# Kernel tuning notes

Hardware: AMD Instinct MI355X
Metric: run time of the kernel (lower is better)

## Reference

```python
import jax, jax.numpy as jnp
import numpy as np

F = 50          # num features
CARD = 10000    # cardinality per feature
D = 64          # factor_dim
A = 64          # attention_size
IU, JU = np.triu_indices(F, k=1)  # upper-triangular pair indices, P = F*(F-1)/2


def setup_inputs() -> dict:
    key = jax.random.key(0)
    ks = jax.random.split(key, 8)
    inputs = jax.random.randint(ks[0], (1024, F), 0, CARD, dtype=jnp.int32)
    emb_table = jax.random.normal(ks[1], (F * CARD, D), dtype=jnp.float32) * 0.05
    w_lin = jax.random.normal(ks[2], (F * CARD,), dtype=jnp.float32) * 0.05
    b_lin = jnp.zeros((1,), dtype=jnp.float32)
    W1 = jax.random.normal(ks[3], (D, A), dtype=jnp.float32) * (1.0 / np.sqrt(D))
    b1 = jnp.zeros((A,), dtype=jnp.float32)
    W2 = jax.random.normal(ks[4], (A, 1), dtype=jnp.float32) * (1.0 / np.sqrt(A))
    b2 = jnp.zeros((1,), dtype=jnp.float32)
    return {"inputs": inputs, "emb_table": emb_table, "w_lin": w_lin,
            "b_lin": b_lin, "W1": W1, "b1": b1, "W2": W2, "b2": b2}


def reference(inputs, emb_table, w_lin, b_lin, W1, b1, W2, b2):
    # Per-feature tables are stacked into one flat table; offset indices per feature.
    flat_idx = inputs + (jnp.arange(F, dtype=jnp.int32) * CARD)[None, :]  # [B, F]
    line_out = jnp.sum(w_lin[flat_idx], axis=1, keepdims=True) + b_lin    # [B, 1]
    factor = emb_table[flat_idx]                                          # [B, F, D]
    # Upper-triangular pairwise element-wise products (i < j), P = F(F-1)/2
    inter = factor[:, IU, :] * factor[:, JU, :]                           # [B, P, D]
    # Attention: Dense(A) -> ReLU -> Dense(1) -> Softmax over pairs
    h = jax.nn.relu(jnp.einsum('bpd,da->bpa', inter, W1) + b1)            # [B, P, A]
    logits = jnp.einsum('bpa,ao->bpo', h, W2) + b2                        # [B, P, 1]
    scores = jax.nn.softmax(logits, axis=1)                               # [B, P, 1]
    pooled = jnp.sum(inter, axis=-1, keepdims=True)                       # [B, P, 1]
    return line_out + jnp.sum(pooled * scores, axis=1)                    # [B, 1]
```

## Files before the change

kernel.cpp:

```cpp
#include <hip/hip_runtime.h>
#include <math.h>

#define FN 50
#define CARD 10000
#define NP 1225
#define NTILE 77
#define NPAD (NTILE*16)
#define FSTRIDE 72

typedef _Float16 half8 __attribute__((ext_vector_type(8)));
typedef __fp16 half2t __attribute__((ext_vector_type(2)));
typedef float floatx4 __attribute__((ext_vector_type(4)));

static __device__ __forceinline__ half2t h2max0(half2t v) {
  half2t r;
  r[0] = v[0] > (__fp16)0 ? v[0] : (__fp16)0;
  r[1] = v[1] > (__fp16)0 ? v[1] : (__fp16)0;
  return r;
}
static __device__ __forceinline__ float hdot2(half2t a, half2t b, float c) {
#if __has_builtin(__builtin_amdgcn_fdot2)
  return __builtin_amdgcn_fdot2(a, b, c, false);
#else
  return c + (float)a[0]*(float)b[0] + (float)a[1]*(float)b[1];
#endif
}

__global__ __launch_bounds__(256, 4)
void afm_kernel(const int* __restrict__ inp,
                const float* __restrict__ emb,
                const float* __restrict__ wlin,
                const float* __restrict__ blin,
                const float* __restrict__ W1,
                const float* __restrict__ b1,
                const float* __restrict__ W2,
                const float* __restrict__ b2,
                float* __restrict__ out)
{
  __shared__ __align__(16) _Float16 s_fac[FN][FSTRIDE];
  __shared__ __align__(16) _Float16 s_w1[512 * 8];
  __shared__ __align__(16) unsigned s_pij[NPAD];
  __shared__ __align__(16) __fp16 s_lg4[NPAD * 4];
  __shared__ float s_pool[NPAD];
  __shared__ float s_wl[FN];
  __shared__ float s_red[16];

  const int tid  = threadIdx.x;
  const int b    = blockIdx.x;
  const int lane = tid & 63;
  const int wave = tid >> 6;
  const int c    = lane & 15;
  const int kq   = lane >> 4;

  for (int p = tid; p < NPAD; p += 256) {
    int pp = p < NP ? p : NP - 1;
    int i = (int)((99.0f - sqrtf(9801.0f - 8.0f * (float)pp)) * 0.5f);
    if (i < 0) i = 0;
    while ((i + 1) * (98 - i) / 2 <= pp) ++i;
    while (i > 0 && i * (99 - i) / 2 > pp) --i;
    int j = pp - i * (99 - i) / 2 + i + 1;
    s_pij[p] = (unsigned)(i * (FSTRIDE * 2)) | ((unsigned)(j * (FSTRIDE * 2)) << 16);
  }

  const int* inprow = inp + b * FN;
  for (int idx = tid; idx < FN * 16; idx += 256) {
    int f = idx >> 4, q = idx & 15;
    int flat = inprow[f] + f * CARD;
    floatx4 v = ((const floatx4*)emb)[(long)flat * 16 + q];
    _Float16* dst = &s_fac[f][q * 4];
    dst[0] = (_Float16)v[0]; dst[1] = (_Float16)v[1];
    dst[2] = (_Float16)v[2]; dst[3] = (_Float16)v[3];
  }
  if (tid < FN) {
    int flat = inprow[tid] + tid * CARD;
    s_wl[tid] = wlin[flat];
  }

  for (int ch = tid; ch < 512; ch += 256) {
    int ks = ch >> 8, mt = (ch >> 6) & 3, ln = ch & 63;
    int cc = ln & 15, kk = ln >> 4;
    _Float16 tmp[8];
#pragma unroll
    for (int j = 0; j < 8; ++j)
      tmp[j] = (_Float16)W1[(ks * 32 + kk * 8 + j) * 64 + mt * 16 + cc];
    *(half8*)&s_w1[ch * 8] = *(const half8*)tmp;
  }

  floatx4 bias[4];
  half2t w2h[4][2];
#pragma unroll
  for (int mt = 0; mt < 4; ++mt) {
    bias[mt] = ((const floatx4*)b1)[mt * 4 + kq];
    floatx4 wv = ((const floatx4*)W2)[mt * 4 + kq];
    w2h[mt][0] = __builtin_amdgcn_cvt_pkrtz(wv[0], wv[1]);
    w2h[mt][1] = __builtin_amdgcn_cvt_pkrtz(wv[2], wv[3]);
  }
  _Float16 onev = (c == 0) ? (_Float16)1 : (_Float16)0;
  half8 onesf = {onev, onev, onev, onev, onev, onev, onev, onev};

  __syncthreads();

#define LDW1(ks, mt) (*(const half8*)&s_w1[(((ks) * 4 + (mt)) * 64 + lane) * 8])
  const char* fbase = (const char*)&s_fac[0][0];
  const int koff = kq * 16;

  int t = wave;
  int pcur = t * 16 + c;
  unsigned po = s_pij[pcur];
  int offi = (int)(po & 0xffffu) + koff;
  int offj = (int)(po >> 16) + koff;
  half8 cvi0 = *(const half8*)(fbase + offi);
  half8 cvj0 = *(const half8*)(fbase + offj);
  half8 cvi1 = *(const half8*)(fbase + offi + 64);
  half8 cvj1 = *(const half8*)(fbase + offj + 64);

  while (true) {
    int tn = t + 4;
    int pn = tn * 16 + c; if (pn > NPAD - 1) pn = NPAD - 1;
    unsigned pon = s_pij[pn];

    half8 pr0 = cvi0 * cvj0;
    half8 pr1 = cvi1 * cvj1;

    floatx4 acc[4];
#pragma unroll
    for (int mt = 0; mt < 4; ++mt) {
      acc[mt] = __builtin_amdgcn_mfma_f32_16x16x32_f16(LDW1(0, mt), pr0, bias[mt], 0, 0, 0);
      acc[mt] = __builtin_amdgcn_mfma_f32_16x16x32_f16(LDW1(1, mt), pr1, acc[mt], 0, 0, 0);
    }
    floatx4 accp = __builtin_amdgcn_mfma_f32_16x16x32_f16(onesf, pr0, (floatx4){0.f,0.f,0.f,0.f}, 0, 0, 0);
    accp = __builtin_amdgcn_mfma_f32_16x16x32_f16(onesf, pr1, accp, 0, 0, 0);

    int offi_n = (int)(pon & 0xffffu) + koff;
    int offj_n = (int)(pon >> 16) + koff;
    cvi0 = *(const half8*)(fbase + offi_n);
    cvj0 = *(const half8*)(fbase + offj_n);
    cvi1 = *(const half8*)(fbase + offi_n + 64);
    cvj1 = *(const half8*)(fbase + offj_n + 64);

    float lg = 0.f;
#pragma unroll
    for (int mt = 0; mt < 4; ++mt) {
      half2t h0 = __builtin_amdgcn_cvt_pkrtz(acc[mt][0], acc[mt][1]);
      half2t h1 = __builtin_amdgcn_cvt_pkrtz(acc[mt][2], acc[mt][3]);
      h0 = h2max0(h0);
      h1 = h2max0(h1);
      lg = hdot2(h0, w2h[mt][0], lg);
      lg = hdot2(h1, w2h[mt][1], lg);
    }
    s_lg4[pcur * 4 + kq] = (__fp16)lg;
    if (kq == 0) s_pool[pcur] = accp[0];

    t = tn;
    if (t >= NTILE) break;
    pcur = t * 16 + c;
  }
#undef LDW1

  __syncthreads();

  float* s_logit = (float*)s_pij;
  float m = -1e30f;
  for (int p = tid; p < NP; p += 256) {
    const half2t* lp = (const half2t*)&s_lg4[p * 4];
    half2t sfh = lp[0] + lp[1];
    float lg = (float)sfh[0] + (float)sfh[1];
    s_logit[p] = lg;
    m = fmaxf(m, lg);
  }
#pragma unroll
  for (int o = 32; o; o >>= 1) m = fmaxf(m, __shfl_xor(m, o, 64));
  if (lane == 0) s_red[wave] = m;
  __syncthreads();
  m = fmaxf(fmaxf(s_red[0], s_red[1]), fmaxf(s_red[2], s_red[3]));
  float se = 0.f, spe = 0.f;
  for (int p = tid; p < NP; p += 256) {
    float e = __expf(s_logit[p] - m);
    se += e;
    spe += e * s_pool[p];
  }
#pragma unroll
  for (int o = 32; o; o >>= 1) {
    se  += __shfl_xor(se, o, 64);
    spe += __shfl_xor(spe, o, 64);
  }
  if (lane == 0) { s_red[4 + wave] = se; s_red[8 + wave] = spe; }
  __syncthreads();
  if (tid == 0) {
    float line = blin[0];
#pragma unroll
    for (int f = 0; f < FN; ++f) line += s_wl[f];
    float SE  = s_red[4] + s_red[5] + s_red[6]  + s_red[7];
    float SPE = s_red[8] + s_red[9] + s_red[10] + s_red[11];
    out[b] = line + SPE / SE;
  }
}

extern "C" void kernel_launch(void* const* d_in, const int* in_sizes, int n_in,
                              void* d_out, int out_size, void* d_ws, size_t ws_size,
                              hipStream_t stream) {
  const int*   inp  = (const int*)d_in[0];
  const float* emb  = (const float*)d_in[1];
  const float* wlin = (const float*)d_in[2];
  const float* blin = (const float*)d_in[3];
  const float* W1   = (const float*)d_in[4];
  const float* b1   = (const float*)d_in[5];
  const float* W2   = (const float*)d_in[6];
  const float* b2   = (const float*)d_in[7];
  float* outp = (float*)d_out;
  const int B = in_sizes[0] / FN;
  afm_kernel<<<B, 256, 0, stream>>>(inp, emb, wlin, blin, W1, b1, W2, b2, outp);
}
```

Before: 24.81 us.

## Hold W1 fragments in registers, compute pool via fdot2, pack logit and pool

```diff
diff --git a/kernel.cpp b/kernel.cpp
--- a/kernel.cpp
+++ b/kernel.cpp
@@ -38,10 +38,8 @@
                 float* __restrict__ out)
 {
   __shared__ __align__(16) _Float16 s_fac[FN][FSTRIDE];
-  __shared__ __align__(16) _Float16 s_w1[512 * 8];
   __shared__ __align__(16) unsigned s_pij[NPAD];
-  __shared__ __align__(16) __fp16 s_lg4[NPAD * 4];
-  __shared__ float s_pool[NPAD];
+  __shared__ __align__(16) half2t  s_lp[NPAD * 4];
   __shared__ float s_wl[FN];
   __shared__ float s_red[16];
 
@@ -76,95 +74,109 @@
     s_wl[tid] = wlin[flat];
   }
 
-  for (int ch = tid; ch < 512; ch += 256) {
-    int ks = ch >> 8, mt = (ch >> 6) & 3, ln = ch & 63;
-    int cc = ln & 15, kk = ln >> 4;
-    _Float16 tmp[8];
-#pragma unroll
-    for (int j = 0; j < 8; ++j)
-      tmp[j] = (_Float16)W1[(ks * 32 + kk * 8 + j) * 64 + mt * 16 + cc];
-    *(half8*)&s_w1[ch * 8] = *(const half8*)tmp;
-  }
-
-  floatx4 bias[4];
-  half2t w2h[4][2];
+  half8 w1f[2][4];
+#pragma unroll
+  for (int ks = 0; ks < 2; ++ks)
+#pragma unroll
+    for (int mt = 0; mt < 4; ++mt)
+#pragma unroll
+      for (int jj = 0; jj < 4; ++jj) {
+        float x = W1[(ks * 32 + kq * 8 + 2 * jj)     * 64 + mt * 16 + c];
+        float y = W1[(ks * 32 + kq * 8 + 2 * jj + 1) * 64 + mt * 16 + c];
+        half2t hw = __builtin_amdgcn_cvt_pkrtz(x, y);
+        w1f[ks][mt][2 * jj]     = (_Float16)hw[0];
+        w1f[ks][mt][2 * jj + 1] = (_Float16)hw[1];
+      }
+  half2t b1h[4][2], w2h[4][2];
 #pragma unroll
   for (int mt = 0; mt < 4; ++mt) {
-    bias[mt] = ((const floatx4*)b1)[mt * 4 + kq];
+    floatx4 bv = ((const floatx4*)b1)[mt * 4 + kq];
     floatx4 wv = ((const floatx4*)W2)[mt * 4 + kq];
+    b1h[mt][0] = __builtin_amdgcn_cvt_pkrtz(bv[0], bv[1]);
+    b1h[mt][1] = __builtin_amdgcn_cvt_pkrtz(bv[2], bv[3]);
     w2h[mt][0] = __builtin_amdgcn_cvt_pkrtz(wv[0], wv[1]);
     w2h[mt][1] = __builtin_amdgcn_cvt_pkrtz(wv[2], wv[3]);
   }
-  _Float16 onev = (c == 0) ? (_Float16)1 : (_Float16)0;
-  half8 onesf = {onev, onev, onev, onev, onev, onev, onev, onev};
-
-  __syncthreads();
-
-#define LDW1(ks, mt) (*(const half8*)&s_w1[(((ks) * 4 + (mt)) * 64 + lane) * 8])
+  const half2t one2 = {(__fp16)1, (__fp16)1};
+
+  __syncthreads();
+
   const char* fbase = (const char*)&s_fac[0][0];
   const int koff = kq * 16;
 
   int t = wave;
   int pcur = t * 16 + c;
-  unsigned po = s_pij[pcur];
-  int offi = (int)(po & 0xffffu) + koff;
-  int offj = (int)(po >> 16) + koff;
-  half8 cvi0 = *(const half8*)(fbase + offi);
-  half8 cvj0 = *(const half8*)(fbase + offj);
-  half8 cvi1 = *(const half8*)(fbase + offi + 64);
-  half8 cvj1 = *(const half8*)(fbase + offj + 64);
-
-  while (true) {
-    int tn = t + 4;
-    int pn = tn * 16 + c; if (pn > NPAD - 1) pn = NPAD - 1;
-    unsigned pon = s_pij[pn];
-
-    half8 pr0 = cvi0 * cvj0;
-    half8 pr1 = cvi1 * cvj1;
-
-    floatx4 acc[4];
-#pragma unroll
-    for (int mt = 0; mt < 4; ++mt) {
-      acc[mt] = __builtin_amdgcn_mfma_f32_16x16x32_f16(LDW1(0, mt), pr0, bias[mt], 0, 0, 0);
-      acc[mt] = __builtin_amdgcn_mfma_f32_16x16x32_f16(LDW1(1, mt), pr1, acc[mt], 0, 0, 0);
+  {
+    unsigned po = s_pij[pcur];
+    int offi = (int)(po & 0xffffu) + koff;
+    int offj = (int)(po >> 16) + koff;
+    half8 cvi0 = *(const half8*)(fbase + offi);
+    half8 cvj0 = *(const half8*)(fbase + offj);
+    half8 cvi1 = *(const half8*)(fbase + offi + 64);
+    half8 cvj1 = *(const half8*)(fbase + offj + 64);
+
+    while (true) {
+      int tn = t + 4;
+      int pn = tn * 16 + c; if (pn > NPAD - 1) pn = NPAD - 1;
+      unsigned pon = s_pij[pn];
+
+      half8 pr0 = cvi0 * cvj0;
+      half8 pr1 = cvi1 * cvj1;
+
+      floatx4 acc[4];
+#pragma unroll
+      for (int mt = 0; mt < 4; ++mt) {
+        acc[mt] = __builtin_amdgcn_mfma_f32_16x16x32_f16(w1f[0][mt], pr0, (floatx4){0.f,0.f,0.f,0.f}, 0, 0, 0);
+        acc[mt] = __builtin_amdgcn_mfma_f32_16x16x32_f16(w1f[1][mt], pr1, acc[mt], 0, 0, 0);
+      }
+
+      const half2t* pp0 = (const half2t*)&pr0;
+      const half2t* pp1 = (const half2t*)&pr1;
+      float pool = 0.f;
+#pragma unroll
+      for (int q = 0; q < 4; ++q) {
+        pool = hdot2(pp0[q], one2, pool);
+        pool = hdot2(pp1[q], one2, pool);
+      }
+
+      int offi_n = (int)(pon & 0xffffu) + koff;
+      int offj_n = (int)(pon >> 16) + koff;
+      cvi0 = *(const half8*)(fbase + offi_n);
+      cvj0 = *(const half8*)(fbase + offj_n);
+      cvi1 = *(const half8*)(fbase + offi_n + 64);
+      cvj1 = *(const half8*)(fbase + offj_n + 64);
+
+      float lg = 0.f;
+#pragma unroll
+      for (int mt = 0; mt < 4; ++mt) {
+        half2t h0 = __builtin_amdgcn_cvt_pkrtz(acc[mt][0], acc[mt][1]);
+        half2t h1 = __builtin_amdgcn_cvt_pkrtz(acc[mt][2], acc[mt][3]);
+        h0 = h2max0(h0 + b1h[mt][0]);
+        h1 = h2max0(h1 + b1h[mt][1]);
+        lg = hdot2(h0, w2h[mt][0], lg);
+        lg = hdot2(h1, w2h[mt][1], lg);
+      }
+      half2t lp;
+      lp[0] = (__fp16)lg;
+      lp[1] = (__fp16)pool;
+      s_lp[pcur * 4 + kq] = lp;
+
+      t = tn;
+      if (t >= NTILE) break;
+      pcur = t * 16 + c;
     }
-    floatx4 accp = __builtin_amdgcn_mfma_f32_16x16x32_f16(onesf, pr0, (floatx4){0.f,0.f,0.f,0.f}, 0, 0, 0);
-    accp = __builtin_amdgcn_mfma_f32_16x16x32_f16(onesf, pr1, accp, 0, 0, 0);
-
-    int offi_n = (int)(pon & 0xffffu) + koff;
-    int offj_n = (int)(pon >> 16) + koff;
-    cvi0 = *(const half8*)(fbase + offi_n);
-    cvj0 = *(const half8*)(fbase + offj_n);
-    cvi1 = *(const half8*)(fbase + offi_n + 64);
-    cvj1 = *(const half8*)(fbase + offj_n + 64);
-
-    float lg = 0.f;
-#pragma unroll
-    for (int mt = 0; mt < 4; ++mt) {
-      half2t h0 = __builtin_amdgcn_cvt_pkrtz(acc[mt][0], acc[mt][1]);
-      half2t h1 = __builtin_amdgcn_cvt_pkrtz(acc[mt][2], acc[mt][3]);
-      h0 = h2max0(h0);
-      h1 = h2max0(h1);
-      lg = hdot2(h0, w2h[mt][0], lg);
-      lg = hdot2(h1, w2h[mt][1], lg);
-    }
-    s_lg4[pcur * 4 + kq] = (__fp16)lg;
-    if (kq == 0) s_pool[pcur] = accp[0];
-
-    t = tn;
-    if (t >= NTILE) break;
-    pcur = t * 16 + c;
-  }
-#undef LDW1
+  }
 
   __syncthreads();
 
   float* s_logit = (float*)s_pij;
+  float* s_poolf = (float*)s_lp;
+  (void)s_poolf;
   float m = -1e30f;
   for (int p = tid; p < NP; p += 256) {
-    const half2t* lp = (const half2t*)&s_lg4[p * 4];
-    half2t sfh = lp[0] + lp[1];
-    float lg = (float)sfh[0] + (float)sfh[1];
+    half2t v0 = s_lp[p * 4 + 0], v1 = s_lp[p * 4 + 1];
+    half2t v2 = s_lp[p * 4 + 2], v3 = s_lp[p * 4 + 3];
+    float lg = (float)v0[0] + (float)v1[0] + (float)v2[0] + (float)v3[0];
     s_logit[p] = lg;
     m = fmaxf(m, lg);
   }
@@ -175,9 +187,12 @@
   m = fmaxf(fmaxf(s_red[0], s_red[1]), fmaxf(s_red[2], s_red[3]));
   float se = 0.f, spe = 0.f;
   for (int p = tid; p < NP; p += 256) {
+    half2t v0 = s_lp[p * 4 + 0], v1 = s_lp[p * 4 + 1];
+    half2t v2 = s_lp[p * 4 + 2], v3 = s_lp[p * 4 + 3];
+    float pool = (float)v0[1] + (float)v1[1] + (float)v2[1] + (float)v3[1];
     float e = __expf(s_logit[p] - m);
     se += e;
-    spe += e * s_pool[p];
+    spe += e * pool;
   }
 #pragma unroll
   for (int o = 32; o; o >>= 1) {
```

Measured after the change: 26.38 us. 6.3% more time.
